# Kernel tuning notes

Measured on AMD Instinct MI355X. Metric: run time of the kernel, lower is better.

Reference implementation:

```python
import jax, jax.numpy as jnp
import numpy as np

N, D_IN, FC_DIM, GROUP, NONGT, EMB = 4096, 12544, 1024, 16, 300, 64
DG = FC_DIM // GROUP  # 64 per-head dim


def extract_position_matrix(bbox, nongt_dim):
    xmin, ymin, xmax, ymax = jnp.split(bbox, 4, axis=1)  # each [N,1]
    bw = xmax - xmin + 1.0
    bh = ymax - ymin + 1.0
    cx = 0.5 * (xmin + xmax)
    cy = 0.5 * (ymin + ymax)
    dx = jnp.log(jnp.maximum(jnp.abs((cx - cx.T) / bw), 1e-3))
    dy = jnp.log(jnp.maximum(jnp.abs((cy - cy.T) / bh), 1e-3))
    dw = jnp.log(bw / bw.T)
    dh = jnp.log(bh / bh.T)
    # slice to first nongt_dim columns, stack -> [N, nongt, 4]
    return jnp.stack([dx[:, :nongt_dim], dy[:, :nongt_dim],
                      dw[:, :nongt_dim], dh[:, :nongt_dim]], axis=2)


def extract_position_embedding(pos_mat, feat_dim=64, wave_length=1000.0):
    n8 = feat_dim // 8
    feat_range = jnp.arange(n8, dtype=pos_mat.dtype)
    dim_mat = wave_length ** (8.0 / feat_dim * feat_range)  # [8]
    div = 100.0 * pos_mat[..., None] / dim_mat              # [N,nongt,4,8]
    emb = jnp.concatenate([jnp.sin(div), jnp.cos(div)], axis=3)  # [N,nongt,4,16]
    return emb.reshape(pos_mat.shape[0], pos_mat.shape[1], feat_dim)


def attention_multi_head(feat, pos_emb, Wpos, bpos, Wq, bq, Wk, bk, Wo, bo):
    # feat: [N, 1024], pos_emb: [N, nongt, 64]
    nongt_feat = feat[:NONGT]                                   # [nongt, 1024]
    aff_w = jax.nn.relu(pos_emb @ Wpos + bpos)                  # [N, nongt, G]
    aff_w = jnp.swapaxes(aff_w, 1, 2)                           # [N, G, nongt]
    q = (feat @ Wq + bq).reshape(-1, GROUP, DG)                 # [N, G, dg]
    k = (nongt_feat @ Wk + bk).reshape(NONGT, GROUP, DG)        # [nongt, G, dg]
    aff = jnp.einsum('ngd,mgd->ngm', q, k) * (1.0 / np.sqrt(DG))  # [N, G, nongt]
    logits = jnp.log(jnp.maximum(aff_w, 1e-6)) + aff
    p = jax.nn.softmax(logits, axis=2)                          # [N, G, nongt]
    out = jnp.einsum('ngm,mc->ngc', p, nongt_feat)              # [N, G, 1024]
    # grouped 1x1 conv: group g maps 1024 -> 64 outputs
    lin = jnp.einsum('ngc,goc->ngo', out, Wo) + bo.reshape(GROUP, DG)
    return lin.reshape(feat.shape[0], FC_DIM)


def setup_inputs() -> dict:
    key = jax.random.key(0)
    ks = jax.random.split(key, 20)
    roi_feat = jax.random.normal(ks[0], (N, D_IN), dtype=jnp.float32)
    u = jax.random.uniform(ks[1], (N, 4), dtype=jnp.float32)
    x1 = u[:, 0:1] * 500.0
    y1 = u[:, 1:2] * 500.0
    bbox = jnp.concatenate([x1, y1, x1 + u[:, 2:3] * 200.0 + 1.0,
                            y1 + u[:, 3:4] * 200.0 + 1.0], axis=1)
    def lin(k, fin, fout):
        s = 1.0 / np.sqrt(fin)
        return jax.random.normal(k, (fin, fout), dtype=jnp.float32) * s
    inp = {'roi_feat': roi_feat, 'bbox': bbox,
           'W_fc1': lin(ks[2], D_IN, FC_DIM), 'b_fc1': jnp.zeros((FC_DIM,), jnp.float32),
           'W_fc2': lin(ks[3], FC_DIM, FC_DIM), 'b_fc2': jnp.zeros((FC_DIM,), jnp.float32)}
    for i, base in [(1, 4), (2, 10)]:
        inp[f'Wpos{i}'] = lin(ks[base], EMB, GROUP)
        inp[f'bpos{i}'] = jnp.zeros((GROUP,), jnp.float32)
        inp[f'Wq{i}'] = lin(ks[base + 1], FC_DIM, FC_DIM)
        inp[f'bq{i}'] = jnp.zeros((FC_DIM,), jnp.float32)
        inp[f'Wk{i}'] = lin(ks[base + 2], FC_DIM, FC_DIM)
        inp[f'bk{i}'] = jnp.zeros((FC_DIM,), jnp.float32)
        inp[f'Wo{i}'] = jax.random.normal(ks[base + 3], (GROUP, DG, FC_DIM), dtype=jnp.float32) * (1.0 / np.sqrt(FC_DIM))
        inp[f'bo{i}'] = jnp.zeros((FC_DIM,), jnp.float32)
    return inp


def reference(roi_feat, bbox, W_fc1, b_fc1, W_fc2, b_fc2,
              Wpos1, bpos1, Wq1, bq1, Wk1, bk1, Wo1, bo1,
              Wpos2, bpos2, Wq2, bq2, Wk2, bk2, Wo2, bo2):
    pos_mat = extract_position_matrix(bbox, NONGT)
    pos_emb = extract_position_embedding(pos_mat, EMB)
    x = roi_feat
    for (Wf, bf, Wp, bp, Wq, bq, Wk, bk, Wo, bo) in [
        (W_fc1, b_fc1, Wpos1, bpos1, Wq1, bq1, Wk1, bk1, Wo1, bo1),
        (W_fc2, b_fc2, Wpos2, bpos2, Wq2, bq2, Wk2, bk2, Wo2, bo2)]:
        x = x @ Wf + bf
        attn = attention_multi_head(x, pos_emb, Wp, bp, Wq, bq, Wk, bk, Wo, bo)
        x = jax.nn.relu(x + attn)
    return x
```

## Files before the change

### kernel.cpp

```cpp
#include <hip/hip_runtime.h>


using bf16x8 = __attribute__((ext_vector_type(8))) short;
using u16x4  = __attribute__((ext_vector_type(4))) short;
using f32x4  = __attribute__((ext_vector_type(4))) float;
typedef unsigned short u16;
typedef unsigned int   u32;

#define DEV __device__ __forceinline__

DEV u16 f2bf(float f) {
  u32 u = __float_as_uint(f);
  return (u16)((u + 0x7FFFu + ((u >> 16) & 1u)) >> 16);
}
DEV float bf2f(u16 h) { return __uint_as_float(((u32)h) << 16); }

DEV f32x4 mfma16(bf16x8 a, bf16x8 b, f32x4 c) {
  return __builtin_amdgcn_mfma_f32_16x16x32_bf16(a, b, c, 0, 0, 0);
}
DEV void gload16(const u16* g, u16* l) {
  __builtin_amdgcn_global_load_lds((const __attribute__((address_space(1))) void*)g,
                                   (__attribute__((address_space(3))) void*)l, 16, 0, 0);
}

DEV void fsincos(float x, float* s, float* c) {
  float r = x * 0.15915494309189535f;
  r -= rintf(r);
  float a = r * 6.283185307179586f;
  *s = __sinf(a); *c = __cosf(a);
}

struct PrepArgs {
  const float* roi; u16* A_b;
  const float* Wo1; u16* Wo1_b;
  const float* Wo2; u16* Wo2_b;
  const float* Wfc1; u16* Wfc1_t;
  const float* wsrc[5]; u16* wdst[5];
};

__global__ __launch_bounds__(256) void prep_kernel(PrepArgs p) {
  __shared__ float tp[32][33];
  int b = blockIdx.x, tid = threadIdx.x;
  if (b < 3072) {
    const float* src; u16* dst; size_t n; int b0, nb;
    if (b < 2048)      { src = p.roi; dst = p.A_b;   n = (size_t)4096 * 12544; b0 = b;        nb = 2048; }
    else if (b < 2560) { src = p.Wo1; dst = p.Wo1_b; n = (size_t)1024 * 1024;  b0 = b - 2048; nb = 512; }
    else               { src = p.Wo2; dst = p.Wo2_b; n = (size_t)1024 * 1024;  b0 = b - 2560; nb = 512; }
    size_t i = ((size_t)b0 * 256 + tid) * 8;
    size_t stride = (size_t)nb * 256 * 8;
    for (; i < n; i += stride) {
      float4 a = *(const float4*)(src + i);
      float4 c = *(const float4*)(src + i + 4);
      bf16x8 v;
      v[0]=(short)f2bf(a.x); v[1]=(short)f2bf(a.y); v[2]=(short)f2bf(a.z); v[3]=(short)f2bf(a.w);
      v[4]=(short)f2bf(c.x); v[5]=(short)f2bf(c.y); v[6]=(short)f2bf(c.z); v[7]=(short)f2bf(c.w);
      *(bf16x8*)(dst + i) = v;
    }
  } else {
    const float* in; u16* out; int r0, c0, R, C;
    if (b < 15616) {
      int idx = b - 3072;
      in = p.Wfc1; out = p.Wfc1_t; R = 12544; C = 1024;
      c0 = (idx & 31) * 32; r0 = (idx >> 5) * 32;
    } else {
      int idx = b - 15616;
      int z = idx >> 10, rest = idx & 1023;
      in = p.wsrc[z]; out = p.wdst[z]; R = 1024; C = 1024;
      c0 = (rest & 31) * 32; r0 = (rest >> 5) * 32;
    }
    int tx = tid & 31, ty = tid >> 5;
#pragma unroll
    for (int i = 0; i < 4; i++)
      tp[ty + i * 8][tx] = in[(size_t)(r0 + ty + i * 8) * C + c0 + tx];
    __syncthreads();
#pragma unroll
    for (int i = 0; i < 4; i++)
      out[(size_t)(c0 + ty + i * 8) * R + r0 + tx] = f2bf(tp[tx][ty + i * 8]);
  }
}

#define WAITBAR(N)                                        \
  asm volatile("s_waitcnt vmcnt(" #N ")" ::: "memory");   \
  __builtin_amdgcn_s_barrier();                           \
  asm volatile("" ::: "memory");

__global__ __launch_bounds__(512, 2) void gemm8p(
    const u16* __restrict__ A, const u16* __restrict__ Bt,
    float* __restrict__ P) {
  const int K = 12544;
  __shared__ u16 lds[65536];
  int tid = threadIdx.x;
  int w = tid >> 6, l = tid & 63, h = l >> 4, l15 = l & 15;
  int wm = w >> 2, wn = w & 3;

  int b = ((blockIdx.x & 7) << 5) | (blockIdx.x >> 3);
  int bz = b >> 6, rest = b & 63;
  int bm = (rest & 15) * 256;
  int bn = (rest >> 4) * 256;
  size_t k0 = (size_t)bz * 3136;

  int X = ((tid >> 3) & 7) << 4;
  int lb = (tid * 16) ^ X;
  int lr = lb >> 7;
  int lc = (lb & 127) >> 1;
  const u16* pA = A + (size_t)(bm + lr) * K + k0 + lc;
  const u16* pB = Bt + (size_t)(bn + lr) * K + k0 + lc;
  const size_t o64 = (size_t)64 * K, o128 = (size_t)128 * K, o192 = (size_t)192 * K;

  int swz = (l15 & 7) << 3;
  int xk0 = (h * 8) ^ swz;
  int xk1 = 32 ^ xk0;
  int rA = (wm * 64 + l15) * 64;
  int rB = (wn * 32 + l15) * 64;

  f32x4 acc[8][4];
#pragma unroll
  for (int i = 0; i < 8; i++)
#pragma unroll
    for (int j = 0; j < 4; j++) acc[i][j] = (f32x4){0.f, 0.f, 0.f, 0.f};

  {
    u16* WA = lds; u16* WB = lds + 16384;
    gload16(pA,        WA + tid * 8);
    gload16(pA + o64,  WA + 4096 + tid * 8);
    gload16(pB,        WB + tid * 8);
    gload16(pB + o64,  WB + 4096 + tid * 8);
    gload16(pB + o128, WB + 8192 + tid * 8);
    gload16(pB + o192, WB + 12288 + tid * 8);
    gload16(pA + o128, WA + 8192 + tid * 8);
    gload16(pA + o192, WA + 12288 + tid * 8);
  }

  bf16x8 af[4][2], bl[2][2], bh[2][2];

#define READ_AF(BASE)                                                    \
  _Pragma("unroll") for (int i = 0; i < 4; i++) {                        \
    af[i][0] = *(const bf16x8*)&LA[(BASE) + rA + i * 1024 + xk0];        \
    af[i][1] = *(const bf16x8*)&LA[(BASE) + rA + i * 1024 + xk1];        \
  }
#define Q_MFMA(QR, QC, BF)                                               \
  __builtin_amdgcn_s_setprio(1);                                         \
  _Pragma("unroll") for (int i = 0; i < 4; i++)                          \
    _Pragma("unroll") for (int j = 0; j < 2; j++) {                      \
      acc[(QR)*4+i][(QC)*2+j] = mfma16(af[i][0], BF[j][0], acc[(QR)*4+i][(QC)*2+j]); \
      acc[(QR)*4+i][(QC)*2+j] = mfma16(af[i][1], BF[j][1], acc[(QR)*4+i][(QC)*2+j]); \
    }                                                                    \
  __builtin_amdgcn_s_setprio(0);

  for (int t = 0; t < 48; t++) {
    const u16* LA = lds + (t & 1) * 32768;
    const u16* LB = LA + 16384;
    u16* WA = lds + ((t + 1) & 1) * 32768;
    u16* WB = WA + 16384;
    int ktn = (t + 1) * 64;
    gload16(pA + ktn,        WA + tid * 8);
    gload16(pA + o64 + ktn,  WA + 4096 + tid * 8);
    WAITBAR(6);
    READ_AF(0);
#pragma unroll
    for (int j = 0; j < 2; j++) {
      bl[j][0] = *(const bf16x8*)&LB[rB + j * 1024 + xk0];
      bl[j][1] = *(const bf16x8*)&LB[rB + j * 1024 + xk1];
    }
    Q_MFMA(0, 0, bl);
    gload16(pB + ktn,        WB + tid * 8);
    gload16(pB + o64 + ktn,  WB + 4096 + tid * 8);
    WAITBAR(6);
#pragma unroll
    for (int j = 0; j < 2; j++) {
      bh[j][0] = *(const bf16x8*)&LB[8192 + rB + j * 1024 + xk0];
      bh[j][1] = *(const bf16x8*)&LB[8192 + rB + j * 1024 + xk1];
    }
    Q_MFMA(0, 1, bh);
    gload16(pB + o128 + ktn, WB + 8192 + tid * 8);
    gload16(pB + o192 + ktn, WB + 12288 + tid * 8);
    gload16(pA + o128 + ktn, WA + 8192 + tid * 8);
    gload16(pA + o192 + ktn, WA + 12288 + tid * 8);
    WAITBAR(8);
    READ_AF(8192);
    Q_MFMA(1, 1, bh);
    Q_MFMA(1, 0, bl);
  }
  {
    const u16* LA = lds;
    const u16* LB = lds + 16384;
    WAITBAR(4);
    READ_AF(0);
#pragma unroll
    for (int j = 0; j < 2; j++) {
      bl[j][0] = *(const bf16x8*)&LB[rB + j * 1024 + xk0];
      bl[j][1] = *(const bf16x8*)&LB[rB + j * 1024 + xk1];
    }
    Q_MFMA(0, 0, bl);
    WAITBAR(2);
#pragma unroll
    for (int j = 0; j < 2; j++) {
      bh[j][0] = *(const bf16x8*)&LB[8192 + rB + j * 1024 + xk0];
      bh[j][1] = *(const bf16x8*)&LB[8192 + rB + j * 1024 + xk1];
    }
    Q_MFMA(0, 1, bh);
    WAITBAR(0);
    READ_AF(8192);
    Q_MFMA(1, 1, bh);
    Q_MFMA(1, 0, bl);
  }
#undef READ_AF
#undef Q_MFMA

  float* dst = P + (size_t)bz * 4096 * 1024;
#pragma unroll
  for (int qr = 0; qr < 2; qr++)
#pragma unroll
    for (int i = 0; i < 4; i++)
#pragma unroll
      for (int qc = 0; qc < 2; qc++)
#pragma unroll
        for (int j = 0; j < 2; j++) {
          int row0 = bm + qr * 128 + wm * 64 + i * 16 + h * 4;
          int col  = bn + qc * 128 + wn * 32 + j * 16 + l15;
          f32x4 v = acc[qr * 4 + i][qc * 2 + j];
#pragma unroll
          for (int r = 0; r < 4; r++)
            dst[(size_t)(row0 + r) * 1024 + col] = v[r];
        }
}

__constant__ float C100D[8] = {100.f, 42.16965034285822f, 17.78279410038923f,
                               7.498942093324559f, 3.1622776601683795f,
                               1.333521432163324f, 0.5623413251903491f,
                               0.23713737056616552f};

__global__ __launch_bounds__(256) void reduce_pos_kernel(
    const float* __restrict__ P, const float* __restrict__ bias,
    float* __restrict__ xf, u16* __restrict__ xb,
    const float* __restrict__ bbox,
    const float* __restrict__ Wpos1, const float* __restrict__ Wpos2,
    const float* __restrict__ bpos1, const float* __restrict__ bpos2,
    u16* __restrict__ logw1, u16* __restrict__ logw2) {
  __shared__ u16 pool[18944];
  int tid = threadIdx.x;
  if (blockIdx.x < 2048) {
    const size_t MN = (size_t)4096 * 1024;
    size_t i = ((size_t)blockIdx.x * 256 + tid) * 4;
    size_t stride = (size_t)2048 * 256 * 4;
    for (; i < MN; i += stride) {
      float4 a = *(const float4*)(P + i);
      float4 b = *(const float4*)(P + MN + i);
      float4 c = *(const float4*)(P + 2 * MN + i);
      float4 d = *(const float4*)(P + 3 * MN + i);
      float4 bv = *(const float4*)(bias + (i & 1023));
      float4 r;
      r.x = a.x + b.x + c.x + d.x + bv.x;
      r.y = a.y + b.y + c.y + d.y + bv.y;
      r.z = a.z + b.z + c.z + d.z + bv.z;
      r.w = a.w + b.w + c.w + d.w + bv.w;
      *(float4*)(xf + i) = r;
      u16x4 hv;
      hv[0] = (short)f2bf(r.x); hv[1] = (short)f2bf(r.y);
      hv[2] = (short)f2bf(r.z); hv[3] = (short)f2bf(r.w);
      *(u16x4*)(xb + i) = hv;
    }
    return;
  }
  u16* emb_s = pool;
  u16* wp_s  = pool + 5632;
  u16* lw_s  = pool + 8448;
  int n = blockIdx.x - 2048;
  int w = tid >> 6, l = tid & 63, h = l >> 4, l15 = l & 15;
  for (int idx = tid; idx < 1024; idx += 256) {
    int e = idx >> 4, c = idx & 15;
    wp_s[c * 88 + e]        = f2bf(Wpos1[idx]);
    wp_s[(16 + c) * 88 + e] = f2bf(Wpos2[idx]);
  }
  float4 bn = ((const float4*)bbox)[n];
  float bw_n = bn.z - bn.x + 1.f, bh_n = bn.w - bn.y + 1.f;
  float cx_n = 0.5f * (bn.x + bn.z), cy_n = 0.5f * (bn.y + bn.w);
  float bps0 = bpos1[l15], bps1 = bpos2[l15];
  int p = tid >> 2, k = tid & 3;

  for (int m0 = 0; m0 < 320; m0 += 64) {
    int m = m0 + p;
    float4 bm = ((const float4*)bbox)[m];
    float v;
    if (k == 0)      v = logf(fmaxf(fabsf((cx_n - 0.5f * (bm.x + bm.z)) / bw_n), 1e-3f));
    else if (k == 1) v = logf(fmaxf(fabsf((cy_n - 0.5f * (bm.y + bm.w)) / bh_n), 1e-3f));
    else if (k == 2) v = logf(bw_n / (bm.z - bm.x + 1.f));
    else             v = logf(bh_n / (bm.w - bm.y + 1.f));
    __syncthreads();
#pragma unroll
    for (int tt = 0; tt < 8; tt++) {
      float s, c; fsincos(v * C100D[tt], &s, &c);
      emb_s[p * 88 + k * 16 + tt]     = f2bf(s);
      emb_s[p * 88 + k * 16 + 8 + tt] = f2bf(c);
    }
    __syncthreads();
    f32x4 acc0 = {0.f, 0.f, 0.f, 0.f}, acc1 = {0.f, 0.f, 0.f, 0.f};
    bf16x8 a0 = *(const bf16x8*)&emb_s[(w * 16 + l15) * 88 + h * 8];
    bf16x8 a1 = *(const bf16x8*)&emb_s[(w * 16 + l15) * 88 + 32 + h * 8];
    bf16x8 b00 = *(const bf16x8*)&wp_s[l15 * 88 + h * 8];
    bf16x8 b01 = *(const bf16x8*)&wp_s[l15 * 88 + 32 + h * 8];
    bf16x8 b10 = *(const bf16x8*)&wp_s[(16 + l15) * 88 + h * 8];
    bf16x8 b11 = *(const bf16x8*)&wp_s[(16 + l15) * 88 + 32 + h * 8];
    acc0 = mfma16(a0, b00, acc0); acc0 = mfma16(a1, b01, acc0);
    acc1 = mfma16(a0, b10, acc1); acc1 = mfma16(a1, b11, acc1);
#pragma unroll
    for (int r = 0; r < 4; r++) {
      int mm = m0 + w * 16 + h * 4 + r;
      lw_s[l15 * 328 + mm]        = f2bf(logf(fmaxf(acc0[r] + bps0, 1e-6f)));
      lw_s[(16 + l15) * 328 + mm] = f2bf(logf(fmaxf(acc1[r] + bps1, 1e-6f)));
    }
  }
  __syncthreads();
  for (int i = tid; i < 1280; i += 256) {
    int layer = i / 640, rest = i - layer * 640;
    int gg = rest / 40, seg = rest - gg * 40;
    bf16x8 v = *(const bf16x8*)&lw_s[(layer * 16 + gg) * 328 + seg * 8];
    u16* dst = (layer ? logw2 : logw1) + ((size_t)gg * 4096 + n) * 320 + seg * 8;
    *(bf16x8*)dst = v;
  }
}

struct GDesc {
  const u16* A; const u16* Bt; const float* bias;
  u16* Cb; float* Cf;
  int M, N, K, ldc, nt;
};

__global__ __launch_bounds__(256, 2) void gemmU(GDesc g0, GDesc g1, GDesc g2,
                                                int c0, int c1) {
  __shared__ u16 lds[32768];
  GDesc g; int lb = blockIdx.x;
  if (lb < c0) { g = g0; lb = (lb & 7) * (c0 >> 3) + (lb >> 3); }
  else if (lb < c1) { g = g1; lb -= c0; }
  else { g = g2; lb -= c1; }
  int bm = (lb / g.nt) * 128, bn = (lb % g.nt) * 128;
  int tid = threadIdx.x;
  int w = tid >> 6, l = tid & 63, h = l >> 4, l15 = l & 15;
  int wm = w >> 1, wn = w & 1;
  int K = g.K;

  int X = ((tid >> 3) & 7) << 4;
  int lbyte = (tid * 16) ^ X;
  int lr = lbyte >> 7, lc = (lbyte & 127) >> 1;
  const u16 *pa[4], *pb[4];
#pragma unroll
  for (int c = 0; c < 4; c++) {
    pa[c] = g.A  + (size_t)min(bm + c * 32 + lr, g.M - 1) * K + lc;
    pb[c] = g.Bt + (size_t)min(bn + c * 32 + lr, g.N - 1) * K + lc;
  }

  int swz = (l15 & 7) << 3;
  int xk0 = (h * 8) ^ swz;
  int xk1 = 32 ^ xk0;
  int rA = (wm * 64 + l15) * 64;
  int rB = (wn * 64 + l15) * 64;

  f32x4 acc[4][4];
#pragma unroll
  for (int i = 0; i < 4; i++)
#pragma unroll
    for (int j = 0; j < 4; j++) acc[i][j] = (f32x4){0.f, 0.f, 0.f, 0.f};

#define ISSUEU(W, kk)                                     \
  { gload16(pa[0] + (kk), (W) + tid * 8);                 \
    gload16(pa[1] + (kk), (W) + 2048 + tid * 8);          \
    gload16(pa[2] + (kk), (W) + 4096 + tid * 8);          \
    gload16(pa[3] + (kk), (W) + 6144 + tid * 8);          \
    gload16(pb[0] + (kk), (W) + 8192 + tid * 8);          \
    gload16(pb[1] + (kk), (W) + 10240 + tid * 8);         \
    gload16(pb[2] + (kk), (W) + 12288 + tid * 8);         \
    gload16(pb[3] + (kk), (W) + 14336 + tid * 8); }

  ISSUEU(lds, 0);
  int ktiles = K >> 6;
  for (int t = 0; t < ktiles; t++) {
    const u16* LA = lds + (t & 1) * 16384;
    const u16* LB = LA + 8192;
    u16* W = lds + ((t ^ 1) & 1) * 16384;
    if (t < ktiles - 1) {
      ISSUEU(W, (t + 1) * 64);
      asm volatile("s_waitcnt vmcnt(8)" ::: "memory");
    } else {
      asm volatile("s_waitcnt vmcnt(0)" ::: "memory");
    }
    __builtin_amdgcn_s_barrier();
    asm volatile("" ::: "memory");
    bf16x8 a[4][2], bfr[4][2];
#pragma unroll
    for (int i = 0; i < 4; i++) {
      a[i][0] = *(const bf16x8*)&LA[rA + i * 1024 + xk0];
      a[i][1] = *(const bf16x8*)&LA[rA + i * 1024 + xk1];
    }
#pragma unroll
    for (int j = 0; j < 4; j++) {
      bfr[j][0] = *(const bf16x8*)&LB[rB + j * 1024 + xk0];
      bfr[j][1] = *(const bf16x8*)&LB[rB + j * 1024 + xk1];
    }
    __builtin_amdgcn_s_setprio(1);
#pragma unroll
    for (int i = 0; i < 4; i++)
#pragma unroll
      for (int j = 0; j < 4; j++) {
        acc[i][j] = mfma16(a[i][0], bfr[j][0], acc[i][j]);
        acc[i][j] = mfma16(a[i][1], bfr[j][1], acc[i][j]);
      }
    __builtin_amdgcn_s_setprio(0);
    asm volatile("" ::: "memory");
    __builtin_amdgcn_s_barrier();
  }
#undef ISSUEU

#pragma unroll
  for (int i = 0; i < 4; i++) {
#pragma unroll
    for (int j = 0; j < 4; j++) {
      int col = bn + wn * 64 + j * 16 + l15;
      if (col >= g.ldc) continue;
      float bv = (g.bias != nullptr && col < g.N) ? g.bias[col] : 0.f;
      int row0 = bm + wm * 64 + i * 16 + h * 4;
#pragma unroll
      for (int r = 0; r < 4; r++) {
        int row = row0 + r;
        if (row >= g.M) continue;
        float v = acc[i][j][r] + bv;
        size_t off = (size_t)row * g.ldc + col;
        g.Cb[off] = f2bf(v);
        if (g.Cf != nullptr) g.Cf[off] = v;
      }
    }
  }
}

template <bool LAST>
__global__ __launch_bounds__(256) void attn_kernel(
    const u16* __restrict__ qb, const u16* __restrict__ kb,
    const u16* __restrict__ kvt, const u16* __restrict__ logw,
    const float* __restrict__ xf, const float* __restrict__ bo,
    float* __restrict__ outf, u16* __restrict__ outb) {
  __shared__ u16 kp_s[320 * 88];
  __shared__ u16 kv_s[64 * 344];
  int tid = threadIdx.x;
  int g = blockIdx.y, n0 = blockIdx.x * 64;
  int w = tid >> 6, l = tid & 63, h = l >> 4, l15 = l & 15;

  for (int i = tid; i < 320 * 8; i += 256) {
    int row = i >> 3, seg = i & 7;
    bf16x8 v = {0, 0, 0, 0, 0, 0, 0, 0};
    if (row < 300) v = *(const bf16x8*)(kb + (size_t)row * 1024 + g * 64 + seg * 8);
    *(bf16x8*)&kp_s[row * 88 + seg * 8] = v;
  }
  for (int i = tid; i < 64 * 40; i += 256) {
    int row = i / 40, seg = i % 40;
    bf16x8 v = *(const bf16x8*)(kvt + (size_t)(g * 64 + row) * 320 + seg * 8);
    *(bf16x8*)&kv_s[row * 344 + seg * 8] = v;
  }
  int nrow = n0 + w * 16 + l15;
  bf16x8 aq0 = *(const bf16x8*)(qb + (size_t)nrow * 1024 + g * 64 + h * 8);
  bf16x8 aq1 = *(const bf16x8*)(qb + (size_t)nrow * 1024 + g * 64 + 32 + h * 8);
  __syncthreads();

  f32x4 acc[19];
#pragma unroll
  for (int f = 0; f < 19; f++) acc[f] = (f32x4){0.f, 0.f, 0.f, 0.f};
#pragma unroll
  for (int f = 0; f < 19; f++) {
    bf16x8 b0 = *(const bf16x8*)&kp_s[(f * 16 + l15) * 88 + h * 8];
    bf16x8 b1 = *(const bf16x8*)&kp_s[(f * 16 + l15) * 88 + 32 + h * 8];
    acc[f] = mfma16(aq0, b0, acc[f]);
    acc[f] = mfma16(aq1, b1, acc[f]);
  }
  __syncthreads();
  {
    const u16* src = logw + ((size_t)g * 4096 + n0) * 320;
    for (int i = tid; i < 64 * 40; i += 256) {
      int row = i / 40, seg = i % 40;
      *(bf16x8*)&kp_s[row * 328 + seg * 8] = *(const bf16x8*)(src + row * 320 + seg * 8);
    }
  }
  __syncthreads();

  int nbase = n0 + w * 16 + h * 4;
  int lrow = w * 16 + h * 4;
  float mx[4] = {-INFINITY, -INFINITY, -INFINITY, -INFINITY};
  float sm[4] = {0.f, 0.f, 0.f, 0.f};
#pragma unroll
  for (int f = 0; f < 19; f++) {
    int m = f * 16 + l15;
#pragma unroll
    for (int r = 0; r < 4; r++) {
      float lw = -INFINITY;
      if (m < 300) lw = bf2f(kp_s[(lrow + r) * 328 + m]);
      float lg = acc[f][r] * 0.125f + lw;
      acc[f][r] = lg;
      mx[r] = fmaxf(mx[r], lg);
    }
  }
#pragma unroll
  for (int d = 1; d < 16; d <<= 1)
#pragma unroll
    for (int r = 0; r < 4; r++) mx[r] = fmaxf(mx[r], __shfl_xor(mx[r], d));
#pragma unroll
  for (int f = 0; f < 19; f++)
#pragma unroll
    for (int r = 0; r < 4; r++) {
      float p = __expf(acc[f][r] - mx[r]);
      acc[f][r] = p; sm[r] += p;
    }
#pragma unroll
  for (int d = 1; d < 16; d <<= 1)
#pragma unroll
    for (int r = 0; r < 4; r++) sm[r] += __shfl_xor(sm[r], d);
  float inv[4];
#pragma unroll
  for (int r = 0; r < 4; r++) inv[r] = 1.f / sm[r];

  __syncthreads();
#pragma unroll
  for (int f = 0; f < 19; f++)
#pragma unroll
    for (int r = 0; r < 4; r++)
      kp_s[(lrow + r) * 344 + f * 16 + l15] = f2bf(acc[f][r]);
#pragma unroll
  for (int r = 0; r < 4; r++)
    kp_s[(lrow + r) * 344 + 304 + l15] = 0;

  f32x4 acc2[4];
#pragma unroll
  for (int fo = 0; fo < 4; fo++) acc2[fo] = (f32x4){0.f, 0.f, 0.f, 0.f};
#pragma unroll
  for (int ks = 0; ks < 10; ks++) {
    bf16x8 ap = *(const bf16x8*)&kp_s[(w * 16 + l15) * 344 + ks * 32 + h * 8];
#pragma unroll
    for (int fo = 0; fo < 4; fo++) {
      bf16x8 bv = *(const bf16x8*)&kv_s[(fo * 16 + l15) * 344 + ks * 32 + h * 8];
      acc2[fo] = mfma16(ap, bv, acc2[fo]);
    }
  }
#pragma unroll
  for (int fo = 0; fo < 4; fo++) {
    int col = g * 64 + fo * 16 + l15;
    float bov = bo[col];
#pragma unroll
    for (int r = 0; r < 4; r++) {
      int row = nbase + r;
      float v = xf[(size_t)row * 1024 + col] + acc2[fo][r] * inv[r] + bov;
      v = fmaxf(v, 0.f);
      if (LAST) outf[(size_t)row * 1024 + col] = v;
      else      outb[(size_t)row * 1024 + col] = f2bf(v);
    }
  }
}

extern "C" void kernel_launch(void* const* d_in, const int* in_sizes, int n_in,
                              void* d_out, int out_size, void* d_ws, size_t ws_size,
                              hipStream_t stream) {
  (void)in_sizes; (void)n_in; (void)out_size; (void)ws_size;
  const float* roi   = (const float*)d_in[0];
  const float* bbox  = (const float*)d_in[1];
  const float* Wfc1  = (const float*)d_in[2];
  const float* bfc1  = (const float*)d_in[3];
  const float* Wfc2  = (const float*)d_in[4];
  const float* bfc2  = (const float*)d_in[5];
  const float* Wpos1 = (const float*)d_in[6];
  const float* bpos1 = (const float*)d_in[7];
  const float* Wq1   = (const float*)d_in[8];
  const float* bq1   = (const float*)d_in[9];
  const float* Wk1   = (const float*)d_in[10];
  const float* bk1   = (const float*)d_in[11];
  const float* Wo1   = (const float*)d_in[12];
  const float* bo1   = (const float*)d_in[13];
  const float* Wpos2 = (const float*)d_in[14];
  const float* bpos2 = (const float*)d_in[15];
  const float* Wq2   = (const float*)d_in[16];
  const float* bq2   = (const float*)d_in[17];
  const float* Wk2   = (const float*)d_in[18];
  const float* bk2   = (const float*)d_in[19];
  const float* Wo2   = (const float*)d_in[20];
  const float* bo2   = (const float*)d_in[21];

  char* ws = (char*)d_ws;
  u16*  A_b    = (u16*)(ws);
  u16*  Wfc1_t = (u16*)(ws + 102760448);
  u16*  Wfc2_t = (u16*)(ws + 128450560);
  u16*  Wq1_t  = (u16*)(ws + 130547712);
  u16*  Wk1_t  = (u16*)(ws + 132644864);
  u16*  Wq2_t  = (u16*)(ws + 134742016);
  u16*  Wk2_t  = (u16*)(ws + 136839168);
  u16*  Wo1_b  = (u16*)(ws + 138936320);
  u16*  Wo2_b  = (u16*)(ws + 141033472);
  float* Pp    = (float*)(ws + 143134720);
  float* xf    = (float*)(ws + 227020800);
  u16*  xb_f   = (u16*)(ws + 243798016);
  u16*  xb_a   = (u16*)(ws + 252186624);
  u16*  q_b    = (u16*)(ws + 260575232);
  u16*  k_b    = (u16*)(ws + 268963840);
  u16*  kvt_b  = (u16*)(ws + 269578240);
  u16*  logw1  = (u16*)(ws + 270233600);
  u16*  logw2  = (u16*)(ws + 312176640);

  {
    PrepArgs p;
    p.roi = roi;   p.A_b = A_b;
    p.Wo1 = Wo1;   p.Wo1_b = Wo1_b;
    p.Wo2 = Wo2;   p.Wo2_b = Wo2_b;
    p.Wfc1 = Wfc1; p.Wfc1_t = Wfc1_t;
    p.wsrc[0] = Wfc2; p.wdst[0] = Wfc2_t;
    p.wsrc[1] = Wq1;  p.wdst[1] = Wq1_t;
    p.wsrc[2] = Wk1;  p.wdst[2] = Wk1_t;
    p.wsrc[3] = Wq2;  p.wdst[3] = Wq2_t;
    p.wsrc[4] = Wk2;  p.wdst[4] = Wk2_t;
    prep_kernel<<<20736, 256, 0, stream>>>(p);
  }
  gemm8p<<<256, 512, 0, stream>>>(A_b, Wfc1_t, Pp);
  reduce_pos_kernel<<<6144, 256, 0, stream>>>(Pp, bfc1, xf, xb_f, bbox,
                                              Wpos1, Wpos2, bpos1, bpos2,
                                              logw1, logw2);
  {
    GDesc q  = {xb_f,  Wq1_t, bq1, q_b,   nullptr, 4096, 1024, 1024, 1024, 8};
    GDesc kk = {xb_f,  Wk1_t, bk1, k_b,   nullptr,  300, 1024, 1024, 1024, 8};
    GDesc kv = {Wo1_b, xb_f,  nullptr, kvt_b, nullptr, 1024, 300, 1024, 320, 3};
    gemmU<<<304, 256, 0, stream>>>(q, kk, kv, 256, 280);
  }
  attn_kernel<false><<<dim3(64, 16), 256, 0, stream>>>(q_b, k_b, kvt_b, logw1, xf, bo1, nullptr, xb_a);

  {
    GDesc fc = {xb_a, Wfc2_t, bfc2, xb_f, xf, 4096, 1024, 1024, 1024, 8};
    gemmU<<<256, 256, 0, stream>>>(fc, fc, fc, 256, 256);
  }
  {
    GDesc q  = {xb_f,  Wq2_t, bq2, q_b,   nullptr, 4096, 1024, 1024, 1024, 8};
    GDesc kk = {xb_f,  Wk2_t, bk2, k_b,   nullptr,  300, 1024, 1024, 1024, 8};
    GDesc kv = {Wo2_b, xb_f,  nullptr, kvt_b, nullptr, 1024, 300, 1024, 320, 3};
    gemmU<<<304, 256, 0, stream>>>(q, kk, kv, 256, 280);
  }
  attn_kernel<true><<<dim3(64, 16), 256, 0, stream>>>(q_b, k_b, kvt_b, logw2, xf, bo2, (float*)d_out, nullptr);
}
```

Baseline: 435.1 us.

## Fuse fp32-to-bf16 conversion of ROI features into the big FC GEMM A-load

Removes the separate pass that converted the 4096x12544 fp32 ROI matrix to bf16 in the workspace. The GEMM now loads fp32 A tiles into registers, converts them and writes swizzled bf16 to LDS, with a simpler one-barrier-per-iteration pipeline. This avoids writing and re-reading about 100MB of intermediate data, at the cost of doubled A global traffic inside the GEMM and register-staged rather than direct-to-LDS loads. The weight-transpose prep is vectorized with float4 reads, and the attention kernel reads K and V straight from global memory instead of staging them in LDS.

```diff
diff --git a/kernel.cpp b/kernel.cpp
--- a/kernel.cpp
+++ b/kernel.cpp
@@ -31,7 +31,6 @@
 }
 
 struct PrepArgs {
-  const float* roi; u16* A_b;
   const float* Wo1; u16* Wo1_b;
   const float* Wo2; u16* Wo2_b;
   const float* Wfc1; u16* Wfc1_t;
@@ -39,53 +38,48 @@
 };
 
 __global__ __launch_bounds__(256) void prep_kernel(PrepArgs p) {
-  __shared__ float tp[32][33];
+  __shared__ float tp[32][36];
   int b = blockIdx.x, tid = threadIdx.x;
-  if (b < 3072) {
-    const float* src; u16* dst; size_t n; int b0, nb;
-    if (b < 2048)      { src = p.roi; dst = p.A_b;   n = (size_t)4096 * 12544; b0 = b;        nb = 2048; }
-    else if (b < 2560) { src = p.Wo1; dst = p.Wo1_b; n = (size_t)1024 * 1024;  b0 = b - 2048; nb = 512; }
-    else               { src = p.Wo2; dst = p.Wo2_b; n = (size_t)1024 * 1024;  b0 = b - 2560; nb = 512; }
-    size_t i = ((size_t)b0 * 256 + tid) * 8;
-    size_t stride = (size_t)nb * 256 * 8;
-    for (; i < n; i += stride) {
-      float4 a = *(const float4*)(src + i);
-      float4 c = *(const float4*)(src + i + 4);
-      bf16x8 v;
-      v[0]=(short)f2bf(a.x); v[1]=(short)f2bf(a.y); v[2]=(short)f2bf(a.z); v[3]=(short)f2bf(a.w);
-      v[4]=(short)f2bf(c.x); v[5]=(short)f2bf(c.y); v[6]=(short)f2bf(c.z); v[7]=(short)f2bf(c.w);
-      *(bf16x8*)(dst + i) = v;
-    }
+  if (b < 1024) {
+    const float* src = (b < 512) ? p.Wo1 : p.Wo2;
+    u16* dst = (b < 512) ? p.Wo1_b : p.Wo2_b;
+    size_t i = ((size_t)(b & 511) * 256 + tid) * 8;
+    float4 a = *(const float4*)(src + i);
+    float4 c = *(const float4*)(src + i + 4);
+    bf16x8 v;
+    v[0]=(short)f2bf(a.x); v[1]=(short)f2bf(a.y); v[2]=(short)f2bf(a.z); v[3]=(short)f2bf(a.w);
+    v[4]=(short)f2bf(c.x); v[5]=(short)f2bf(c.y); v[6]=(short)f2bf(c.z); v[7]=(short)f2bf(c.w);
+    *(bf16x8*)(dst + i) = v;
+    return;
+  }
+  const float* in; u16* out; int r0, c0, R, C;
+  if (b < 13568) {
+    int idx = b - 1024;
+    in = p.Wfc1; out = p.Wfc1_t; R = 12544; C = 1024;
+    r0 = (idx >> 5) * 32; c0 = (idx & 31) * 32;
   } else {
-    const float* in; u16* out; int r0, c0, R, C;
-    if (b < 15616) {
-      int idx = b - 3072;
-      in = p.Wfc1; out = p.Wfc1_t; R = 12544; C = 1024;
-      c0 = (idx & 31) * 32; r0 = (idx >> 5) * 32;
-    } else {
-      int idx = b - 15616;
-      int z = idx >> 10, rest = idx & 1023;
-      in = p.wsrc[z]; out = p.wdst[z]; R = 1024; C = 1024;
-      c0 = (rest & 31) * 32; r0 = (rest >> 5) * 32;
-    }
-    int tx = tid & 31, ty = tid >> 5;
-#pragma unroll
-    for (int i = 0; i < 4; i++)
-      tp[ty + i * 8][tx] = in[(size_t)(r0 + ty + i * 8) * C + c0 + tx];
-    __syncthreads();
-#pragma unroll
-    for (int i = 0; i < 4; i++)
-      out[(size_t)(c0 + ty + i * 8) * R + r0 + tx] = f2bf(tp[tx][ty + i * 8]);
-  }
-}
-
-#define WAITBAR(N)                                        \
-  asm volatile("s_waitcnt vmcnt(" #N ")" ::: "memory");   \
-  __builtin_amdgcn_s_barrier();                           \
-  asm volatile("" ::: "memory");
+    int idx = b - 13568;
+    int z = idx >> 10, rest = idx & 1023;
+    in = p.wsrc[z]; out = p.wdst[z]; R = 1024; C = 1024;
+    r0 = (rest >> 5) * 32; c0 = (rest & 31) * 32;
+  }
+  {
+    int r = tid >> 3, c4 = (tid & 7) * 4;
+    float4 v = *(const float4*)(in + (size_t)(r0 + r) * C + c0 + c4);
+    *(float4*)&tp[r][c4] = v;
+  }
+  __syncthreads();
+  {
+    int c = tid >> 3, r4 = (tid & 7) * 4;
+    u16x4 o;
+    o[0] = (short)f2bf(tp[r4 + 0][c]); o[1] = (short)f2bf(tp[r4 + 1][c]);
+    o[2] = (short)f2bf(tp[r4 + 2][c]); o[3] = (short)f2bf(tp[r4 + 3][c]);
+    *(u16x4*)(out + (size_t)(c0 + c) * R + r0 + r4) = o;
+  }
+}
 
 __global__ __launch_bounds__(512, 2) void gemm8p(
-    const u16* __restrict__ A, const u16* __restrict__ Bt,
+    const float* __restrict__ A, const u16* __restrict__ Bt,
     float* __restrict__ P) {
   const int K = 12544;
   __shared__ u16 lds[65536];
@@ -99,11 +93,17 @@
   int bn = (rest >> 4) * 256;
   size_t k0 = (size_t)bz * 3136;
 
+  int arow = tid >> 3;
+  int c0e = (tid & 7) * 4;
+  const float* pA0 = A + (size_t)(bm + arow) * K + k0 + c0e;
+  const float* pA1 = pA0 + 32;
+  const size_t aseg = (size_t)64 * K;
+  int awe0 = ((arow * 128 + c0e * 2) ^ ((arow & 7) << 4)) >> 1;
+  int awe1 = ((arow * 128 + 64 + c0e * 2) ^ ((arow & 7) << 4)) >> 1;
+
   int X = ((tid >> 3) & 7) << 4;
-  int lb = (tid * 16) ^ X;
-  int lr = lb >> 7;
-  int lc = (lb & 127) >> 1;
-  const u16* pA = A + (size_t)(bm + lr) * K + k0 + lc;
+  int lb2 = (tid * 16) ^ X;
+  int lr = lb2 >> 7, lc = (lb2 & 127) >> 1;
   const u16* pB = Bt + (size_t)(bn + lr) * K + k0 + lc;
   const size_t o64 = (size_t)64 * K, o128 = (size_t)128 * K, o192 = (size_t)192 * K;
 
@@ -119,20 +119,25 @@
 #pragma unroll
     for (int j = 0; j < 4; j++) acc[i][j] = (f32x4){0.f, 0.f, 0.f, 0.f};
 
-  {
-    u16* WA = lds; u16* WB = lds + 16384;
-    gload16(pA,        WA + tid * 8);
-    gload16(pA + o64,  WA + 4096 + tid * 8);
-    gload16(pB,        WB + tid * 8);
-    gload16(pB + o64,  WB + 4096 + tid * 8);
-    gload16(pB + o128, WB + 8192 + tid * 8);
-    gload16(pB + o192, WB + 12288 + tid * 8);
-    gload16(pA + o128, WA + 8192 + tid * 8);
-    gload16(pA + o192, WA + 12288 + tid * 8);
-  }
-
+  float4 a0[4], a1[4];
   bf16x8 af[4][2], bl[2][2], bh[2][2];
 
+#define AISSUE(kk) { _Pragma("unroll") for (int s = 0; s < 4; s++) {     \
+    a0[s] = *(const float4*)(pA0 + s * aseg + (kk));                     \
+    a1[s] = *(const float4*)(pA1 + s * aseg + (kk)); } }
+#define BISSUE(WB, kk) {                                                 \
+    gload16(pB + (kk),        (WB) + tid * 8);                           \
+    gload16(pB + o64 + (kk),  (WB) + 4096 + tid * 8);                    \
+    gload16(pB + o128 + (kk), (WB) + 8192 + tid * 8);                    \
+    gload16(pB + o192 + (kk), (WB) + 12288 + tid * 8); }
+#define AWRITE(WA) { _Pragma("unroll") for (int s = 0; s < 4; s++) {     \
+    u16x4 v0, v1;                                                        \
+    v0[0]=(short)f2bf(a0[s].x); v0[1]=(short)f2bf(a0[s].y);              \
+    v0[2]=(short)f2bf(a0[s].z); v0[3]=(short)f2bf(a0[s].w);              \
+    v1[0]=(short)f2bf(a1[s].x); v1[1]=(short)f2bf(a1[s].y);              \
+    v1[2]=(short)f2bf(a1[s].z); v1[3]=(short)f2bf(a1[s].w);              \
+    *(u16x4*)&(WA)[awe0 + s * 4096] = v0;                                \
+    *(u16x4*)&(WA)[awe1 + s * 4096] = v1; } }
 #define READ_AF(BASE)                                                    \
   _Pragma("unroll") for (int i = 0; i < 4; i++) {                        \
     af[i][0] = *(const bf16x8*)&LA[(BASE) + rA + i * 1024 + xk0];        \
@@ -147,15 +152,23 @@
     }                                                                    \
   __builtin_amdgcn_s_setprio(0);
 
-  for (int t = 0; t < 48; t++) {
+  AISSUE(0);
+  BISSUE(lds + 16384, 0);
+  AWRITE(lds);
+  asm volatile("s_waitcnt vmcnt(0) lgkmcnt(0)" ::: "memory");
+  __builtin_amdgcn_s_barrier();
+
+  for (int t = 0; t < 49; t++) {
     const u16* LA = lds + (t & 1) * 32768;
     const u16* LB = LA + 16384;
     u16* WA = lds + ((t + 1) & 1) * 32768;
     u16* WB = WA + 16384;
-    int ktn = (t + 1) * 64;
-    gload16(pA + ktn,        WA + tid * 8);
-    gload16(pA + o64 + ktn,  WA + 4096 + tid * 8);
-    WAITBAR(6);
+    if (t < 48) {
+      int ktn = (t + 1) * 64;
+      AISSUE(ktn);
+      BISSUE(WB, ktn);
+    }
+    __builtin_amdgcn_sched_barrier(0);
     READ_AF(0);
 #pragma unroll
     for (int j = 0; j < 2; j++) {
@@ -163,47 +176,27 @@
       bl[j][1] = *(const bf16x8*)&LB[rB + j * 1024 + xk1];
     }
     Q_MFMA(0, 0, bl);
-    gload16(pB + ktn,        WB + tid * 8);
-    gload16(pB + o64 + ktn,  WB + 4096 + tid * 8);
-    WAITBAR(6);
+    __builtin_amdgcn_sched_barrier(0);
 #pragma unroll
     for (int j = 0; j < 2; j++) {
       bh[j][0] = *(const bf16x8*)&LB[8192 + rB + j * 1024 + xk0];
       bh[j][1] = *(const bf16x8*)&LB[8192 + rB + j * 1024 + xk1];
     }
     Q_MFMA(0, 1, bh);
-    gload16(pB + o128 + ktn, WB + 8192 + tid * 8);
-    gload16(pB + o192 + ktn, WB + 12288 + tid * 8);
-    gload16(pA + o128 + ktn, WA + 8192 + tid * 8);
-    gload16(pA + o192 + ktn, WA + 12288 + tid * 8);
-    WAITBAR(8);
+    __builtin_amdgcn_sched_barrier(0);
     READ_AF(8192);
     Q_MFMA(1, 1, bh);
+    __builtin_amdgcn_sched_barrier(0);
     Q_MFMA(1, 0, bl);
-  }
-  {
-    const u16* LA = lds;
-    const u16* LB = lds + 16384;
-    WAITBAR(4);
-    READ_AF(0);
-#pragma unroll
-    for (int j = 0; j < 2; j++) {
-      bl[j][0] = *(const bf16x8*)&LB[rB + j * 1024 + xk0];
-      bl[j][1] = *(const bf16x8*)&LB[rB + j * 1024 + xk1];
-    }
-    Q_MFMA(0, 0, bl);
-    WAITBAR(2);
-#pragma unroll
-    for (int j = 0; j < 2; j++) {
-      bh[j][0] = *(const bf16x8*)&LB[8192 + rB + j * 1024 + xk0];
-      bh[j][1] = *(const bf16x8*)&LB[8192 + rB + j * 1024 + xk1];
-    }
-    Q_MFMA(0, 1, bh);
-    WAITBAR(0);
-    READ_AF(8192);
-    Q_MFMA(1, 1, bh);
-    Q_MFMA(1, 0, bl);
-  }
+    __builtin_amdgcn_sched_barrier(0);
+    if (t < 48) { AWRITE(WA); }
+    asm volatile("s_waitcnt vmcnt(0) lgkmcnt(0)" ::: "memory");
+    __builtin_amdgcn_sched_barrier(0);
+    __builtin_amdgcn_s_barrier();
+  }
+#undef AISSUE
+#undef BISSUE
+#undef AWRITE
 #undef READ_AF
 #undef Q_MFMA
 
@@ -437,45 +430,33 @@
     const u16* __restrict__ kvt, const u16* __restrict__ logw,
     const float* __restrict__ xf, const float* __restrict__ bo,
     float* __restrict__ outf, u16* __restrict__ outb) {
-  __shared__ u16 kp_s[320 * 88];
-  __shared__ u16 kv_s[64 * 344];
+  __shared__ u16 ps[64 * 344];
   int tid = threadIdx.x;
   int g = blockIdx.y, n0 = blockIdx.x * 64;
   int w = tid >> 6, l = tid & 63, h = l >> 4, l15 = l & 15;
 
-  for (int i = tid; i < 320 * 8; i += 256) {
-    int row = i >> 3, seg = i & 7;
-    bf16x8 v = {0, 0, 0, 0, 0, 0, 0, 0};
-    if (row < 300) v = *(const bf16x8*)(kb + (size_t)row * 1024 + g * 64 + seg * 8);
-    *(bf16x8*)&kp_s[row * 88 + seg * 8] = v;
-  }
-  for (int i = tid; i < 64 * 40; i += 256) {
-    int row = i / 40, seg = i % 40;
-    bf16x8 v = *(const bf16x8*)(kvt + (size_t)(g * 64 + row) * 320 + seg * 8);
-    *(bf16x8*)&kv_s[row * 344 + seg * 8] = v;
-  }
-  int nrow = n0 + w * 16 + l15;
-  bf16x8 aq0 = *(const bf16x8*)(qb + (size_t)nrow * 1024 + g * 64 + h * 8);
-  bf16x8 aq1 = *(const bf16x8*)(qb + (size_t)nrow * 1024 + g * 64 + 32 + h * 8);
-  __syncthreads();
-
-  f32x4 acc[19];
-#pragma unroll
-  for (int f = 0; f < 19; f++) acc[f] = (f32x4){0.f, 0.f, 0.f, 0.f};
-#pragma unroll
-  for (int f = 0; f < 19; f++) {
-    bf16x8 b0 = *(const bf16x8*)&kp_s[(f * 16 + l15) * 88 + h * 8];
-    bf16x8 b1 = *(const bf16x8*)&kp_s[(f * 16 + l15) * 88 + 32 + h * 8];
-    acc[f] = mfma16(aq0, b0, acc[f]);
-    acc[f] = mfma16(aq1, b1, acc[f]);
-  }
-  __syncthreads();
   {
     const u16* src = logw + ((size_t)g * 4096 + n0) * 320;
     for (int i = tid; i < 64 * 40; i += 256) {
-      int row = i / 40, seg = i % 40;
-      *(bf16x8*)&kp_s[row * 328 + seg * 8] = *(const bf16x8*)(src + row * 320 + seg * 8);
-    }
+      int row = i / 40, seg = i - row * 40;
+      *(bf16x8*)&ps[row * 328 + seg * 8] = *(const bf16x8*)(src + row * 320 + seg * 8);
+    }
+  }
+  int nrow = n0 + w * 16 + l15;
+  const u16* qp = qb + (size_t)nrow * 1024 + g * 64;
+  bf16x8 aq0 = *(const bf16x8*)(qp + h * 8);
+  bf16x8 aq1 = *(const bf16x8*)(qp + 32 + h * 8);
+
+  f32x4 acc[19];
+#pragma unroll
+  for (int f = 0; f < 19; f++) acc[f] = (f32x4){0.f, 0.f, 0.f, 0.f};
+  const u16* kp = kb + g * 64 + h * 8;
+#pragma unroll
+  for (int f = 0; f < 19; f++) {
+    bf16x8 b0 = *(const bf16x8*)(kp + (size_t)(f * 16 + l15) * 1024);
+    bf16x8 b1 = *(const bf16x8*)(kp + (size_t)(f * 16 + l15) * 1024 + 32);
+    acc[f] = mfma16(aq0, b0, acc[f]);
+    acc[f] = mfma16(aq1, b1, acc[f]);
   }
   __syncthreads();
 
@@ -489,7 +470,7 @@
 #pragma unroll
     for (int r = 0; r < 4; r++) {
       float lw = -INFINITY;
-      if (m < 300) lw = bf2f(kp_s[(lrow + r) * 328 + m]);
+      if (m < 300) lw = bf2f(ps[(lrow + r) * 328 + m]);
       float lg = acc[f][r] * 0.125f + lw;
       acc[f][r] = lg;
       mx[r] = fmaxf(mx[r], lg);
@@ -519,20 +500,21 @@
   for (int f = 0; f < 19; f++)
 #pragma unroll
     for (int r = 0; r < 4; r++)
-      kp_s[(lrow + r) * 344 + f * 16 + l15] = f2bf(acc[f][r]);
+      ps[(lrow + r) * 344 + f * 16 + l15] = f2bf(acc[f][r]);
 #pragma unroll
   for (int r = 0; r < 4; r++)
-    kp_s[(lrow + r) * 344 + 304 + l15] = 0;
+    ps[(lrow + r) * 344 + 304 + l15] = 0;
 
   f32x4 acc2[4];
 #pragma unroll
   for (int fo = 0; fo < 4; fo++) acc2[fo] = (f32x4){0.f, 0.f, 0.f, 0.f};
+  const u16* vp = kvt + (size_t)g * 64 * 320 + h * 8;
 #pragma unroll
   for (int ks = 0; ks < 10; ks++) {
-    bf16x8 ap = *(const bf16x8*)&kp_s[(w * 16 + l15) * 344 + ks * 32 + h * 8];
+    bf16x8 ap = *(const bf16x8*)&ps[(w * 16 + l15) * 344 + ks * 32 + h * 8];
 #pragma unroll
     for (int fo = 0; fo < 4; fo++) {
-      bf16x8 bv = *(const bf16x8*)&kv_s[(fo * 16 + l15) * 344 + ks * 32 + h * 8];
+      bf16x8 bv = *(const bf16x8*)(vp + (size_t)(fo * 16 + l15) * 320 + ks * 32);
       acc2[fo] = mfma16(ap, bv, acc2[fo]);
     }
   }
@@ -579,7 +561,6 @@
   const float* bo2   = (const float*)d_in[21];
 
   char* ws = (char*)d_ws;
-  u16*  A_b    = (u16*)(ws);
   u16*  Wfc1_t = (u16*)(ws + 102760448);
   u16*  Wfc2_t = (u16*)(ws + 128450560);
   u16*  Wq1_t  = (u16*)(ws + 130547712);
@@ -600,7 +581,6 @@
 
   {
     PrepArgs p;
-    p.roi = roi;   p.A_b = A_b;
     p.Wo1 = Wo1;   p.Wo1_b = Wo1_b;
     p.Wo2 = Wo2;   p.Wo2_b = Wo2_b;
     p.Wfc1 = Wfc1; p.Wfc1_t = Wfc1_t;
@@ -609,9 +589,9 @@
     p.wsrc[2] = Wk1;  p.wdst[2] = Wk1_t;
     p.wsrc[3] = Wq2;  p.wdst[3] = Wq2_t;
     p.wsrc[4] = Wk2;  p.wdst[4] = Wk2_t;
-    prep_kernel<<<20736, 256, 0, stream>>>(p);
-  }
-  gemm8p<<<256, 512, 0, stream>>>(A_b, Wfc1_t, Pp);
+    prep_kernel<<<18688, 256, 0, stream>>>(p);
+  }
+  gemm8p<<<256, 512, 0, stream>>>(roi, Wfc1_t, Pp);
   reduce_pos_kernel<<<6144, 256, 0, stream>>>(Pp, bfc1, xf, xb_f, bbox,
                                               Wpos1, Wpos2, bpos1, bpos2,
                                               logw1, logw2);
```

Measured after the change: 425.7 us. 2.2% less time.
